# Optimization experiments

Measured on AMD Instinct MI355X. Metric: run time of the kernel, lower is better.

## Reference

```python
import jax, jax.numpy as jnp
import numpy as np

EPS = 1e-12  # F.normalize default eps


def setup_inputs() -> dict:
    key = jax.random.key(0)
    x = jax.random.normal(key, (4, 64, 8192, 1), dtype=jnp.float32)
    return {"x": x, "k": 9, "dilation": 1}


def reference(x, k, dilation):
    # x: (B, D, N, 1)
    B, D, N, _ = x.shape
    kk = k * dilation
    # F.normalize(x, p=2, dim=1)
    norm = jnp.linalg.norm(x, axis=1, keepdims=True)
    xn = x / jnp.maximum(norm, EPS)
    # -> (B, N, D)
    pts = jnp.squeeze(xn, -1).transpose(0, 2, 1)
    # pairwise euclidean distance (cdist p=2)
    sq = jnp.sum(pts * pts, axis=-1)  # (B, N)
    d2 = sq[:, :, None] + sq[:, None, :] - 2.0 * jnp.einsum("bnd,bmd->bnm", pts, pts)
    dist = jnp.sqrt(jnp.maximum(d2, 0.0))  # (B, N, N)
    # torch.topk(-dist, k): k smallest distances
    _, nn_idx = jax.lax.top_k(-dist, kk)  # (B, N, kk)
    center_idx = jnp.broadcast_to(jnp.arange(N, dtype=nn_idx.dtype)[None, :, None], (B, N, kk))
    edge_index = jnp.stack([nn_idx, center_idx], axis=0)  # (2, B, N, kk)
    return edge_index[:, :, :, ::dilation]
```

## Files before the change

### kernel.cpp

```cpp
#include <hip/hip_runtime.h>

#define BB 4
#define DD 64
#define NN 8192
#define KK 9


typedef __attribute__((ext_vector_type(8))) _Float16 f16x8;
typedef __attribute__((ext_vector_type(16))) float f32x16;

__device__ __forceinline__ uint4 pack8(const unsigned* w) {
    return make_uint4(w[0] | (w[1] << 16), w[2] | (w[3] << 16),
                      w[4] | (w[5] << 16), w[6] | (w[7] << 16));
}

__device__ __forceinline__ float min3f(float a, float b, float c) {
    return fminf(fminf(a, b), c);
}

__global__ __launch_bounds__(256) void knorm2_kernel(const float* __restrict__ x,
                                                     float* __restrict__ xnT,
                                                     float* __restrict__ sq,
                                                     unsigned short* __restrict__ Phi,
                                                     unsigned short* __restrict__ Shi) {
    int t = blockIdx.x * 256 + threadIdx.x;
    int b = t >> 13;
    int n = t & (NN - 1);
    const float* xb = x + (size_t)b * DD * NN + n;
    float v[DD];
    float ss = 0.0f;
#pragma unroll
    for (int d = 0; d < DD; ++d) {
        v[d] = xb[(size_t)d * NN];
        ss = fmaf(v[d], v[d], ss);
    }
    float inv = 1.0f / fmaxf(sqrtf(ss), 1e-12f);
    float s2 = 0.0f;
#pragma unroll
    for (int d = 0; d < DD; ++d) {
        v[d] *= inv;
        s2 = fmaf(v[d], v[d], s2);
    }
    sq[t] = s2;
    float4* o4 = reinterpret_cast<float4*>(xnT + (size_t)t * DD);
#pragma unroll
    for (int d = 0; d < DD; d += 4) o4[d >> 2] = make_float4(v[d], v[d+1], v[d+2], v[d+3]);

    size_t base = (size_t)t * DD;
#pragma unroll
    for (int d0 = 0; d0 < DD; d0 += 8) {
        unsigned ph[8], sh[8];
#pragma unroll
        for (int e = 0; e < 8; ++e) {
            float f = v[d0 + e];
            _Float16 hp = (_Float16)f;
            _Float16 hs = (_Float16)(-2.0f * f);
            ph[e] = (unsigned)__builtin_bit_cast(unsigned short, hp);
            sh[e] = (unsigned)__builtin_bit_cast(unsigned short, hs);
        }
        *reinterpret_cast<uint4*>(Phi + base + d0) = pack8(ph);
        *reinterpret_cast<uint4*>(Shi + base + d0) = pack8(sh);
    }
}

__global__ __launch_bounds__(256, 4) void kmin_kernel(const unsigned short* __restrict__ Shi,
                                                      const unsigned short* __restrict__ Phi,
                                                      float* __restrict__ minbuf) {
    __shared__ float stage[4][64][33];
    const int lane = threadIdx.x & 63;
    const int wave = threadIdx.x >> 6;
    const int l31 = lane & 31;
    const int half = lane >> 5;
    const int i0 = blockIdx.x * 256 + wave * 64;
    const int b = i0 >> 13;
    const int jloc0 = blockIdx.y * (NN / 8);
    const int goff = jloc0 >> 5;

    f16x8 Bh0[4], Bh1[4];
    {
        const size_t ib0 = (size_t)(i0 + l31) * DD + half * 8;
        const size_t ib1 = (size_t)(i0 + 32 + l31) * DD + half * 8;
#pragma unroll
        for (int kc = 0; kc < 4; ++kc) {
            Bh0[kc] = *reinterpret_cast<const f16x8*>(Phi + ib0 + kc * 16);
            Bh1[kc] = *reinterpret_cast<const f16x8*>(Phi + ib1 + kc * 16);
        }
    }
    const size_t ja0 = ((size_t)b * NN + jloc0 + l31) * DD + half * 8;

#pragma unroll 1
    for (int f = 0; f < 2; ++f) {
#pragma unroll 2
        for (int u = 0; u < 16; ++u) {
            const int tt = f * 16 + u;
            const size_t ja = ja0 + (size_t)tt * 32 * DD;
            f16x8 Ah[4];
#pragma unroll
            for (int kc = 0; kc < 4; ++kc)
                Ah[kc] = *reinterpret_cast<const f16x8*>(Shi + ja + kc * 16);
            f32x16 c0 = {}, c1 = {};
#pragma unroll
            for (int kc = 0; kc < 4; ++kc)
                c0 = __builtin_amdgcn_mfma_f32_32x32x16_f16(Ah[kc], Bh0[kc], c0, 0, 0, 0);
#pragma unroll
            for (int kc = 0; kc < 4; ++kc)
                c1 = __builtin_amdgcn_mfma_f32_32x32x16_f16(Ah[kc], Bh1[kc], c1, 0, 0, 0);
            {
                float t0 = min3f(c0[0], c0[1], c0[2]);
                float t1 = min3f(c0[3], c0[4], c0[5]);
                float t2 = min3f(c0[6], c0[7], c0[8]);
                float t3 = min3f(c0[9], c0[10], c0[11]);
                float t4 = min3f(c0[12], c0[13], c0[14]);
                stage[wave][l31][half * 16 + u] =
                    fminf(min3f(t0, t1, t2), min3f(t3, t4, c0[15]));
            }
            {
                float t0 = min3f(c1[0], c1[1], c1[2]);
                float t1 = min3f(c1[3], c1[4], c1[5]);
                float t2 = min3f(c1[6], c1[7], c1[8]);
                float t3 = min3f(c1[9], c1[10], c1[11]);
                float t4 = min3f(c1[12], c1[13], c1[14]);
                stage[wave][32 + l31][half * 16 + u] =
                    fminf(min3f(t0, t1, t2), min3f(t3, t4, c1[15]));
            }
        }
        const int gbase = goff + f * 16;
#pragma unroll
        for (int it = 0; it < 8; ++it) {
            int idx = it * 64 + lane;
            int c4 = idx & 3;
            int hf = (idx >> 2) & 1;
            int r = idx >> 3;
            const float* s = &stage[wave][r][hf * 16 + c4 * 4];
            float4 vv = make_float4(s[0], s[1], s[2], s[3]);
            *reinterpret_cast<float4*>(minbuf + (size_t)(i0 + r) * 512 +
                                       hf * 256 + gbase + c4 * 4) = vv;
        }
    }
}

__global__ __launch_bounds__(256) void ksel_kernel(const float* __restrict__ xnT,
                                                   const float* __restrict__ sq,
                                                   const float* __restrict__ minbuf,
                                                   const unsigned short* __restrict__ Phi,
                                                   int* __restrict__ out) {
    __shared__ unsigned short glist[4][40];
    __shared__ unsigned short jlist[4][64];
    const int lane = threadIdx.x & 63;
    const int wave = threadIdx.x >> 6;
    const int t = blockIdx.x * 4 + wave;
    const int tu = __builtin_amdgcn_readfirstlane(t);
    const int b = tu >> 13;
    const int n = tu & (NN - 1);

    float gm[8];
    {
        const float4* m4 = reinterpret_cast<const float4*>(minbuf + (size_t)tu * 512 + lane * 8);
        float4 a = m4[0], c = m4[1];
        gm[0] = a.x; gm[1] = a.y; gm[2] = a.z; gm[3] = a.w;
        gm[4] = c.x; gm[5] = c.y; gm[6] = c.z; gm[7] = c.w;
    }

    float sv = fminf(min3f(gm[0], gm[1], gm[2]),
                     fminf(min3f(gm[3], gm[4], gm[5]), fminf(gm[6], gm[7])));
#pragma unroll
    for (int k = 2; k <= 64; k <<= 1) {
#pragma unroll
        for (int jj = k >> 1; jj >= 1; jj >>= 1) {
            float o = __shfl_xor(sv, jj);
            bool keepMin = (((lane & jj) == 0) == ((lane & k) == 0));
            sv = keepMin ? fminf(sv, o) : fmaxf(sv, o);
        }
    }
    const float th9p = __shfl(sv, 8);
    const float theta  = th9p + 8e-3f;
    const float kappa1 = th9p + 5.5e-3f;

    int cnt = 0;
    unsigned short* gl = &glist[wave][0];
#pragma unroll
    for (int q = 0; q < 8; ++q) {
        bool c = gm[q] <= theta;
        unsigned long long mask = __ballot(c);
        int pos = cnt + __popcll(mask & ((1ULL << lane) - 1ULL));
        if (c && pos < 40) gl[pos] = (unsigned short)(lane * 8 + q);
        cnt += (int)__popcll(mask);
    }
    __syncthreads();

    const float* __restrict__ Bb = xnT + (size_t)b * NN * DD;
    const float* __restrict__ sqb = sq + (size_t)b * NN;
    const unsigned short* __restrict__ Pb = Phi + ((size_t)b * NN) * DD;
    float ar[DD];
    {
        const float4* a4 = reinterpret_cast<const float4*>(xnT + (size_t)tu * DD);
#pragma unroll
        for (int d = 0; d < DD; d += 4) {
            float4 f = a4[d >> 2];
            ar[d] = f.x; ar[d + 1] = f.y; ar[d + 2] = f.z; ar[d + 3] = f.w;
        }
    }

    const bool ovf = (cnt > 40);
    const int total = ovf ? NN : cnt * 16;
    const int nIt = (total + 63) >> 6;
    int S1 = 0;
    unsigned short* jl = &jlist[wave][0];
#pragma unroll 1
    for (int m = 0; m < nIt; ++m) {
        const int idx = m * 64 + lane;
        const bool act = idx < total;
        float m2ap = __uint_as_float(0x7f800000u);
        int j = 0;
        if (act) {
            if (ovf) {
                j = idx;
            } else {
                int g = (int)gl[idx >> 4];
                int s4 = idx & 15;
                j = (g & 255) * 32 + ((s4 >> 2) * 8) + ((g >> 8) * 4) + (s4 & 3);
            }
            const f16x8* p8 = reinterpret_cast<const f16x8*>(Pb + (size_t)j * DD);
            float a0 = 0.0f, a1 = 0.0f, a2 = 0.0f, a3 = 0.0f;
#pragma unroll
            for (int c8 = 0; c8 < 8; ++c8) {
                f16x8 h = p8[c8];
                a0 = fmaf((float)h[0], ar[c8 * 8 + 0], a0);
                a1 = fmaf((float)h[1], ar[c8 * 8 + 1], a1);
                a2 = fmaf((float)h[2], ar[c8 * 8 + 2], a2);
                a3 = fmaf((float)h[3], ar[c8 * 8 + 3], a3);
                a0 = fmaf((float)h[4], ar[c8 * 8 + 4], a0);
                a1 = fmaf((float)h[5], ar[c8 * 8 + 5], a1);
                a2 = fmaf((float)h[6], ar[c8 * 8 + 6], a2);
                a3 = fmaf((float)h[7], ar[c8 * 8 + 7], a3);
            }
            m2ap = -2.0f * ((a0 + a1) + (a2 + a3));
        }
        bool pass = act && (m2ap <= kappa1);
        unsigned long long mask = __ballot(pass);
        int pos = S1 + __popcll(mask & ((1ULL << lane) - 1ULL));
        if (pass && pos < 64) jl[pos] = (unsigned short)j;
        S1 += (int)__popcll(mask);
    }
    __syncthreads();

    unsigned long long kout = ~0ULL;
    if (S1 <= 64) {
        unsigned long long v = ~0ULL;
        if (lane < S1) {
            int j = (int)jl[lane];
            const float4* bc4 = reinterpret_cast<const float4*>(Bb + (size_t)j * DD);
            float a0 = 0.0f, a1 = 0.0f, a2 = 0.0f, a3 = 0.0f;
#pragma unroll
            for (int d4 = 0; d4 < DD / 4; ++d4) {
                float4 f = bc4[d4];
                a0 = fmaf(ar[4 * d4 + 0], f.x, a0);
                a1 = fmaf(ar[4 * d4 + 1], f.y, a1);
                a2 = fmaf(ar[4 * d4 + 2], f.z, a2);
                a3 = fmaf(ar[4 * d4 + 3], f.w, a3);
            }
            float dot = (a0 + a1) + (a2 + a3);
            float key = fmaf(-2.0f, dot, sqb[j]);
            unsigned ub = __float_as_uint(key);
            ub ^= (0x80000000u | (unsigned)((int)ub >> 31));
            v = ((unsigned long long)ub << 32) | (unsigned)j;
        }
#pragma unroll
        for (int k = 2; k <= 64; k <<= 1) {
#pragma unroll
            for (int jj = k >> 1; jj >= 1; jj >>= 1) {
                unsigned long long o = __shfl_xor(v, jj);
                bool keepMin = (((lane & jj) == 0) == ((lane & k) == 0));
                bool less = o < v;
                unsigned long long mn = less ? o : v;
                unsigned long long mx = less ? v : o;
                v = keepMin ? mn : mx;
            }
        }
        kout = v;
    } else {
        unsigned long long kd[KK];
#pragma unroll
        for (int m = 0; m < KK; ++m) kd[m] = ~0ULL;
#pragma unroll 1
        for (int m = 0; m < nIt; ++m) {
            const int idx = m * 64 + lane;
            if (idx >= total) continue;
            int j;
            if (ovf) {
                j = idx;
            } else {
                int g = (int)gl[idx >> 4];
                int s4 = idx & 15;
                j = (g & 255) * 32 + ((s4 >> 2) * 8) + ((g >> 8) * 4) + (s4 & 3);
            }
            const float4* bc4 = reinterpret_cast<const float4*>(Bb + (size_t)j * DD);
            float a0 = 0.0f, a1 = 0.0f, a2 = 0.0f, a3 = 0.0f;
#pragma unroll
            for (int d4 = 0; d4 < DD / 4; ++d4) {
                float4 f = bc4[d4];
                a0 = fmaf(ar[4 * d4 + 0], f.x, a0);
                a1 = fmaf(ar[4 * d4 + 1], f.y, a1);
                a2 = fmaf(ar[4 * d4 + 2], f.z, a2);
                a3 = fmaf(ar[4 * d4 + 3], f.w, a3);
            }
            float dot = (a0 + a1) + (a2 + a3);
            float key = fmaf(-2.0f, dot, sqb[j]);
            unsigned ub = __float_as_uint(key);
            ub ^= (0x80000000u | (unsigned)((int)ub >> 31));
            unsigned long long cnd = ((unsigned long long)ub << 32) | (unsigned)j;
            if (cnd < kd[KK - 1]) {
#pragma unroll
                for (int m2 = 0; m2 < KK; ++m2) {
                    bool sw = cnd < kd[m2];
                    unsigned long long lo = sw ? cnd : kd[m2];
                    unsigned long long hi = sw ? kd[m2] : cnd;
                    kd[m2] = lo;
                    cnd = hi;
                }
            }
        }
#pragma unroll
        for (int r = 0; r < KK; ++r) {
            unsigned long long c = kd[0];
            unsigned long long wm = c;
#pragma unroll
            for (int d = 1; d < 64; d <<= 1) {
                unsigned long long o = __shfl_xor(wm, d);
                wm = (o < wm) ? o : wm;
            }
            if (lane == r) kout = wm;
            if (c == wm) {
#pragma unroll
                for (int m2 = 0; m2 < KK - 1; ++m2) kd[m2] = kd[m2 + 1];
                kd[KK - 1] = ~0ULL;
            }
        }
    }

    if (lane < KK) {
        out[(size_t)tu * KK + lane] = (int)(kout & 0xFFFFFFFFULL);
        out[(size_t)BB * NN * KK + (size_t)tu * KK + lane] = n;
    }
}

__global__ __launch_bounds__(256) void knorm_kernel(const float* __restrict__ x,
                                                    float* __restrict__ xnT,
                                                    float* __restrict__ sq) {
    int t = blockIdx.x * 256 + threadIdx.x;
    int b = t >> 13;
    int n = t & (NN - 1);
    const float* xb = x + (size_t)b * DD * NN + n;
    float v[DD];
    float ss = 0.0f;
#pragma unroll
    for (int d = 0; d < DD; ++d) {
        v[d] = xb[(size_t)d * NN];
        ss = fmaf(v[d], v[d], ss);
    }
    float norm = sqrtf(ss);
    float inv = 1.0f / fmaxf(norm, 1e-12f);
    float s2 = 0.0f;
#pragma unroll
    for (int d = 0; d < DD; ++d) {
        float xv = v[d] * inv;
        v[d] = xv;
        s2 = fmaf(xv, xv, s2);
    }
    float4* o4 = reinterpret_cast<float4*>(xnT + (size_t)t * DD);
#pragma unroll
    for (int d = 0; d < DD; d += 4) {
        o4[d >> 2] = make_float4(v[d], v[d + 1], v[d + 2], v[d + 3]);
    }
    sq[t] = s2;
}

template <int S>
__global__ __launch_bounds__(256, 2) void kdist_kernel(const float* __restrict__ xnT,
                                                       const float* __restrict__ sq,
                                                       unsigned long long* __restrict__ cand) {
    const int rb = blockIdx.x;
    const int b = rb >> 5;
    const int nbase = (rb & 31) * 256;
    const int n = nbase + threadIdx.x;
    const int s = blockIdx.y;
    const int jcount = NN / S;
    const int j0 = s * jcount;
    const int j1 = j0 + jcount;

    const float* __restrict__ Bb = xnT + ((size_t)b * NN) * DD;
    const float* __restrict__ sqb = sq + (size_t)b * NN;

    float ar[DD];
    {
        const float4* a4 = reinterpret_cast<const float4*>(Bb + (size_t)n * DD);
#pragma unroll
        for (int d = 0; d < DD; d += 4) {
            float4 f = a4[d >> 2];
            ar[d] = f.x; ar[d + 1] = f.y; ar[d + 2] = f.z; ar[d + 3] = f.w;
        }
    }
#pragma unroll
    for (int d = 0; d < DD; ++d) {
        asm volatile("" : "+v"(ar[d]));
    }

    unsigned long long kd[KK];
#pragma unroll
    for (int m = 0; m < KK; ++m) kd[m] = ~0ULL;

#pragma unroll 2
    for (int j = j0; j < j1; ++j) {
        const float4* bc4 = reinterpret_cast<const float4*>(Bb + (size_t)j * DD);
        float a0 = 0.0f, a1 = 0.0f, a2 = 0.0f, a3 = 0.0f;
#pragma unroll
        for (int d4 = 0; d4 < DD / 4; ++d4) {
            float4 f = bc4[d4];
            a0 = fmaf(ar[4 * d4 + 0], f.x, a0);
            a1 = fmaf(ar[4 * d4 + 1], f.y, a1);
            a2 = fmaf(ar[4 * d4 + 2], f.z, a2);
            a3 = fmaf(ar[4 * d4 + 3], f.w, a3);
        }
        float dot = (a0 + a1) + (a2 + a3);
        float key = fmaf(-2.0f, dot, sqb[j]);
        unsigned int ub = __float_as_uint(key);
        ub ^= (0x80000000u | (unsigned int)((int)ub >> 31));
        unsigned long long cnd = ((unsigned long long)ub << 32) | (unsigned int)j;
        if (cnd < kd[KK - 1]) {
#pragma unroll
            for (int m = 0; m < KK; ++m) {
                bool sw = cnd < kd[m];
                unsigned long long lo = sw ? cnd : kd[m];
                unsigned long long hi = sw ? kd[m] : cnd;
                kd[m] = lo;
                cnd = hi;
            }
        }
    }

    unsigned long long* outc = cand + ((size_t)(b * NN + n) * S + s) * KK;
#pragma unroll
    for (int m = 0; m < KK; ++m) outc[m] = kd[m];
}

template <int S>
__global__ __launch_bounds__(256) void kmerge_kernel(const unsigned long long* __restrict__ cand,
                                                     int* __restrict__ out) {
    int t = blockIdx.x * 256 + threadIdx.x;
    const unsigned long long* c = cand + (size_t)t * (S * KK);
    unsigned long long kd[KK];
#pragma unroll
    for (int m = 0; m < KK; ++m) kd[m] = ~0ULL;
#pragma unroll
    for (int q = 0; q < S * KK; ++q) {
        unsigned long long cnd = c[q];
        if (cnd < kd[KK - 1]) {
#pragma unroll
            for (int m = 0; m < KK; ++m) {
                bool sw = cnd < kd[m];
                unsigned long long lo = sw ? cnd : kd[m];
                unsigned long long hi = sw ? kd[m] : cnd;
                kd[m] = lo;
                cnd = hi;
            }
        }
    }
    int n = t & (NN - 1);
    int* out0 = out + (size_t)t * KK;
    int* out1 = out + (size_t)BB * NN * KK + (size_t)t * KK;
#pragma unroll
    for (int m = 0; m < KK; ++m) {
        out0[m] = (int)(kd[m] & 0xFFFFFFFFULL);
        out1[m] = n;
    }
}

extern "C" void kernel_launch(void* const* d_in, const int* in_sizes, int n_in,
                              void* d_out, int out_size, void* d_ws, size_t ws_size,
                              hipStream_t stream) {
    const float* x = (const float*)d_in[0];
    int* out = (int*)d_out;
    char* ws = (char*)d_ws;

    constexpr size_t XNT_B = (size_t)BB * NN * DD * 4;
    constexpr size_t SQ_B  = (size_t)BB * NN * 4;
    float* xnT = (float*)ws;
    float* sq  = (float*)(ws + XNT_B);

    constexpr size_t BF_B  = (size_t)BB * NN * DD * 2;
    constexpr size_t OFF_PHI = XNT_B + SQ_B;
    constexpr size_t OFF_PLO = OFF_PHI + BF_B;
    constexpr size_t OFF_SHI = OFF_PLO + BF_B;
    constexpr size_t OFF_SLO = OFF_SHI + BF_B;
    constexpr size_t OFF_MIN = OFF_SLO + BF_B;
    constexpr size_t MIN_B   = (size_t)512 * BB * NN * 4;
    constexpr size_t NEED_NEW = OFF_MIN + MIN_B;

    if (ws_size >= NEED_NEW) {
        unsigned short* Phi = (unsigned short*)(ws + OFF_PHI);
        unsigned short* Shi = (unsigned short*)(ws + OFF_SHI);
        float* minbuf = (float*)(ws + OFF_MIN);

        knorm2_kernel<<<dim3(BB * NN / 256), dim3(256), 0, stream>>>(x, xnT, sq, Phi, Shi);
        kmin_kernel<<<dim3(BB * NN / 256, 8), dim3(256), 0, stream>>>(Shi, Phi, minbuf);
        ksel_kernel<<<dim3(BB * NN / 4), dim3(256), 0, stream>>>(xnT, sq, minbuf, Phi, out);
        return;
    }

    unsigned long long* cand = (unsigned long long*)(ws + XNT_B + SQ_B);
    const size_t base = XNT_B + SQ_B;
    const size_t need8 = base + (size_t)BB * NN * 8 * KK * 8;

    knorm_kernel<<<dim3(BB * NN / 256), dim3(256), 0, stream>>>(x, xnT, sq);
    if (ws_size >= need8) {
        kdist_kernel<8><<<dim3(BB * NN / 256, 8), dim3(256), 0, stream>>>(xnT, sq, cand);
        kmerge_kernel<8><<<dim3(BB * NN / 256), dim3(256), 0, stream>>>(cand, out);
    } else {
        kdist_kernel<4><<<dim3(BB * NN / 256, 4), dim3(256), 0, stream>>>(xnT, sq, cand);
        kmerge_kernel<4><<<dim3(BB * NN / 256), dim3(256), 0, stream>>>(cand, out);
    }
}
```

Before: 249.3 us.

## Double-buffer A-tile loads in MFMA min kernel and use fdot2 in selection filter

The min-distance kernel now flattens its two-phase loop and double-buffers the A-operand fragments, so the next tile's global loads are issued while the current tile's MFMAs and min reductions run. The selection kernel's approximate filter now computes dot products with packed fp16 fdot2 instructions, using an fp16 copy of the query row, in place of per-element float conversions and FMAs. The full-precision query row is loaded only after the filter loop, which should shorten register live ranges. The filter margin kappa1 is widened to absorb the extra fp16 rounding, which may let more candidates through to the exact pass and raises overflow risk.

```diff
diff --git a/kernel.cpp b/kernel.cpp
--- a/kernel.cpp
+++ b/kernel.cpp
@@ -8,6 +8,8 @@
 
 typedef __attribute__((ext_vector_type(8))) _Float16 f16x8;
 typedef __attribute__((ext_vector_type(16))) float f32x16;
+typedef __attribute__((ext_vector_type(2))) _Float16 h2;
+struct H2x4 { h2 a, b, c, d; };
 
 __device__ __forceinline__ uint4 pack8(const unsigned* w) {
     return make_uint4(w[0] | (w[1] << 16), w[2] | (w[3] << 16),
@@ -16,6 +18,15 @@
 
 __device__ __forceinline__ float min3f(float a, float b, float c) {
     return fminf(fminf(a, b), c);
+}
+
+__device__ __forceinline__ float dot2acc(h2 g, h2 r, float acc) {
+#if __has_builtin(__builtin_amdgcn_fdot2)
+    return __builtin_amdgcn_fdot2(g, r, acc, false);
+#else
+    acc = fmaf((float)g[0], (float)r[0], acc);
+    return fmaf((float)g[1], (float)r[1], acc);
+#endif
 }
 
 __global__ __launch_bounds__(256) void knorm2_kernel(const float* __restrict__ x,
@@ -88,53 +99,92 @@
     }
     const size_t ja0 = ((size_t)b * NN + jloc0 + l31) * DD + half * 8;
 
-#pragma unroll 1
-    for (int f = 0; f < 2; ++f) {
+    f16x8 A0[4], A1[4];
+#pragma unroll
+    for (int kc = 0; kc < 4; ++kc)
+        A0[kc] = *reinterpret_cast<const f16x8*>(Shi + ja0 + kc * 16);
+
 #pragma unroll 2
-        for (int u = 0; u < 16; ++u) {
-            const int tt = f * 16 + u;
-            const size_t ja = ja0 + (size_t)tt * 32 * DD;
-            f16x8 Ah[4];
+    for (int u2 = 0; u2 < 16; ++u2) {
+        const int t0 = u2 * 2;
+        {
+            const size_t ja = ja0 + (size_t)(t0 + 1) * 32 * DD;
 #pragma unroll
             for (int kc = 0; kc < 4; ++kc)
-                Ah[kc] = *reinterpret_cast<const f16x8*>(Shi + ja + kc * 16);
+                A1[kc] = *reinterpret_cast<const f16x8*>(Shi + ja + kc * 16);
+        }
+        {
             f32x16 c0 = {}, c1 = {};
 #pragma unroll
             for (int kc = 0; kc < 4; ++kc)
-                c0 = __builtin_amdgcn_mfma_f32_32x32x16_f16(Ah[kc], Bh0[kc], c0, 0, 0, 0);
+                c0 = __builtin_amdgcn_mfma_f32_32x32x16_f16(A0[kc], Bh0[kc], c0, 0, 0, 0);
 #pragma unroll
             for (int kc = 0; kc < 4; ++kc)
-                c1 = __builtin_amdgcn_mfma_f32_32x32x16_f16(Ah[kc], Bh1[kc], c1, 0, 0, 0);
+                c1 = __builtin_amdgcn_mfma_f32_32x32x16_f16(A0[kc], Bh1[kc], c1, 0, 0, 0);
+            const int col = half * 16 + (t0 & 15);
             {
-                float t0 = min3f(c0[0], c0[1], c0[2]);
-                float t1 = min3f(c0[3], c0[4], c0[5]);
-                float t2 = min3f(c0[6], c0[7], c0[8]);
-                float t3 = min3f(c0[9], c0[10], c0[11]);
-                float t4 = min3f(c0[12], c0[13], c0[14]);
-                stage[wave][l31][half * 16 + u] =
-                    fminf(min3f(t0, t1, t2), min3f(t3, t4, c0[15]));
+                float q0 = min3f(c0[0], c0[1], c0[2]);
+                float q1 = min3f(c0[3], c0[4], c0[5]);
+                float q2 = min3f(c0[6], c0[7], c0[8]);
+                float q3 = min3f(c0[9], c0[10], c0[11]);
+                float q4 = min3f(c0[12], c0[13], c0[14]);
+                stage[wave][l31][col] = fminf(min3f(q0, q1, q2), min3f(q3, q4, c0[15]));
             }
             {
-                float t0 = min3f(c1[0], c1[1], c1[2]);
-                float t1 = min3f(c1[3], c1[4], c1[5]);
-                float t2 = min3f(c1[6], c1[7], c1[8]);
-                float t3 = min3f(c1[9], c1[10], c1[11]);
-                float t4 = min3f(c1[12], c1[13], c1[14]);
-                stage[wave][32 + l31][half * 16 + u] =
-                    fminf(min3f(t0, t1, t2), min3f(t3, t4, c1[15]));
-            }
-        }
-        const int gbase = goff + f * 16;
-#pragma unroll
-        for (int it = 0; it < 8; ++it) {
-            int idx = it * 64 + lane;
-            int c4 = idx & 3;
-            int hf = (idx >> 2) & 1;
-            int r = idx >> 3;
-            const float* s = &stage[wave][r][hf * 16 + c4 * 4];
-            float4 vv = make_float4(s[0], s[1], s[2], s[3]);
-            *reinterpret_cast<float4*>(minbuf + (size_t)(i0 + r) * 512 +
-                                       hf * 256 + gbase + c4 * 4) = vv;
+                float q0 = min3f(c1[0], c1[1], c1[2]);
+                float q1 = min3f(c1[3], c1[4], c1[5]);
+                float q2 = min3f(c1[6], c1[7], c1[8]);
+                float q3 = min3f(c1[9], c1[10], c1[11]);
+                float q4 = min3f(c1[12], c1[13], c1[14]);
+                stage[wave][32 + l31][col] = fminf(min3f(q0, q1, q2), min3f(q3, q4, c1[15]));
+            }
+        }
+        if (u2 < 15) {
+            const size_t ja = ja0 + (size_t)(t0 + 2) * 32 * DD;
+#pragma unroll
+            for (int kc = 0; kc < 4; ++kc)
+                A0[kc] = *reinterpret_cast<const f16x8*>(Shi + ja + kc * 16);
+        }
+        {
+            f32x16 c0 = {}, c1 = {};
+#pragma unroll
+            for (int kc = 0; kc < 4; ++kc)
+                c0 = __builtin_amdgcn_mfma_f32_32x32x16_f16(A1[kc], Bh0[kc], c0, 0, 0, 0);
+#pragma unroll
+            for (int kc = 0; kc < 4; ++kc)
+                c1 = __builtin_amdgcn_mfma_f32_32x32x16_f16(A1[kc], Bh1[kc], c1, 0, 0, 0);
+            const int col = half * 16 + ((t0 + 1) & 15);
+            {
+                float q0 = min3f(c0[0], c0[1], c0[2]);
+                float q1 = min3f(c0[3], c0[4], c0[5]);
+                float q2 = min3f(c0[6], c0[7], c0[8]);
+                float q3 = min3f(c0[9], c0[10], c0[11]);
+                float q4 = min3f(c0[12], c0[13], c0[14]);
+                stage[wave][l31][col] = fminf(min3f(q0, q1, q2), min3f(q3, q4, c0[15]));
+            }
+            {
+                float q0 = min3f(c1[0], c1[1], c1[2]);
+                float q1 = min3f(c1[3], c1[4], c1[5]);
+                float q2 = min3f(c1[6], c1[7], c1[8]);
+                float q3 = min3f(c1[9], c1[10], c1[11]);
+                float q4 = min3f(c1[12], c1[13], c1[14]);
+                stage[wave][32 + l31][col] = fminf(min3f(q0, q1, q2), min3f(q3, q4, c1[15]));
+            }
+        }
+        if ((t0 & 15) == 14) {
+            const int f = t0 >> 4;
+            const int gbase = goff + f * 16;
+#pragma unroll
+            for (int it = 0; it < 8; ++it) {
+                int idx = it * 64 + lane;
+                int c4 = idx & 3;
+                int hf = (idx >> 2) & 1;
+                int r = idx >> 3;
+                const float* s = &stage[wave][r][hf * 16 + c4 * 4];
+                float4 vv = make_float4(s[0], s[1], s[2], s[3]);
+                *reinterpret_cast<float4*>(minbuf + (size_t)(i0 + r) * 512 +
+                                           hf * 256 + gbase + c4 * 4) = vv;
+            }
         }
     }
 }
@@ -174,7 +224,7 @@
     }
     const float th9p = __shfl(sv, 8);
     const float theta  = th9p + 8e-3f;
-    const float kappa1 = th9p + 5.5e-3f;
+    const float kappa1 = th9p + 6.5e-3f;
 
     int cnt = 0;
     unsigned short* gl = &glist[wave][0];
@@ -188,17 +238,12 @@
     }
     __syncthreads();
 
-    const float* __restrict__ Bb = xnT + (size_t)b * NN * DD;
-    const float* __restrict__ sqb = sq + (size_t)b * NN;
     const unsigned short* __restrict__ Pb = Phi + ((size_t)b * NN) * DD;
-    float ar[DD];
+    H2x4 arh[8];
     {
-        const float4* a4 = reinterpret_cast<const float4*>(xnT + (size_t)tu * DD);
-#pragma unroll
-        for (int d = 0; d < DD; d += 4) {
-            float4 f = a4[d >> 2];
-            ar[d] = f.x; ar[d + 1] = f.y; ar[d + 2] = f.z; ar[d + 3] = f.w;
-        }
+        const f16x8* pr = reinterpret_cast<const f16x8*>(Phi + (size_t)tu * DD);
+#pragma unroll
+        for (int c8 = 0; c8 < 8; ++c8) arh[c8] = __builtin_bit_cast(H2x4, pr[c8]);
     }
 
     const bool ovf = (cnt > 40);
@@ -224,15 +269,11 @@
             float a0 = 0.0f, a1 = 0.0f, a2 = 0.0f, a3 = 0.0f;
 #pragma unroll
             for (int c8 = 0; c8 < 8; ++c8) {
-                f16x8 h = p8[c8];
-                a0 = fmaf((float)h[0], ar[c8 * 8 + 0], a0);
-                a1 = fmaf((float)h[1], ar[c8 * 8 + 1], a1);
-                a2 = fmaf((float)h[2], ar[c8 * 8 + 2], a2);
-                a3 = fmaf((float)h[3], ar[c8 * 8 + 3], a3);
-                a0 = fmaf((float)h[4], ar[c8 * 8 + 4], a0);
-                a1 = fmaf((float)h[5], ar[c8 * 8 + 5], a1);
-                a2 = fmaf((float)h[6], ar[c8 * 8 + 6], a2);
-                a3 = fmaf((float)h[7], ar[c8 * 8 + 7], a3);
+                H2x4 g2 = __builtin_bit_cast(H2x4, p8[c8]);
+                a0 = dot2acc(g2.a, arh[c8].a, a0);
+                a1 = dot2acc(g2.b, arh[c8].b, a1);
+                a2 = dot2acc(g2.c, arh[c8].c, a2);
+                a3 = dot2acc(g2.d, arh[c8].d, a3);
             }
             m2ap = -2.0f * ((a0 + a1) + (a2 + a3));
         }
@@ -243,6 +284,18 @@
         S1 += (int)__popcll(mask);
     }
     __syncthreads();
+
+    const float* __restrict__ Bb = xnT + (size_t)b * NN * DD;
+    const float* __restrict__ sqb = sq + (size_t)b * NN;
+    float ar[DD];
+    {
+        const float4* a4 = reinterpret_cast<const float4*>(xnT + (size_t)tu * DD);
+#pragma unroll
+        for (int d = 0; d < DD; d += 4) {
+            float4 f = a4[d >> 2];
+            ar[d] = f.x; ar[d + 1] = f.y; ar[d + 2] = f.z; ar[d + 3] = f.w;
+        }
+    }
 
     unsigned long long kout = ~0ULL;
     if (S1 <= 64) {
```

New measurement: 247.4 us. No clear change (-0.8%).
